# Performance work log

Measured on AMD Instinct MI355X. Metric: run time of the kernel, lower is better.

Reference implementation:

```python
import jax, jax.numpy as jnp
import numpy as np

N_NODES = 100000
N_EDGES = 3200000
IN_FEATS = 512
N_HIDDEN = 64
N_CLASSES = 16
K_HOPS = 10
ALPHA = 0.1


def setup_inputs() -> dict:
    key = jax.random.key(0)
    ks = jax.random.split(key, 6)
    feature = jax.random.normal(ks[0], (N_NODES, IN_FEATS), dtype=jnp.float32)
    W1 = jax.random.normal(ks[1], (IN_FEATS, N_HIDDEN), dtype=jnp.float32) / np.sqrt(IN_FEATS)
    b1 = jnp.zeros((N_HIDDEN,), dtype=jnp.float32)
    W2 = jax.random.normal(ks[2], (N_HIDDEN, N_CLASSES), dtype=jnp.float32) / np.sqrt(N_HIDDEN)
    b2 = jnp.zeros((N_CLASSES,), dtype=jnp.float32)
    edge_index = jax.random.randint(ks[3], (2, N_EDGES), 0, N_NODES, dtype=jnp.int64)
    # normalized edge weights ~ 1/avg_degree to keep propagation stable
    norm_A = jax.random.uniform(ks[4], (N_EDGES,), dtype=jnp.float32) * (2.0 / 32.0)
    # GPR coefficients: gamma_k = alpha*(1-alpha)^k, gamma_K = (1-alpha)^K
    kk = jnp.arange(K_HOPS + 1, dtype=jnp.float32)
    temp = ALPHA * (1.0 - ALPHA) ** kk
    temp = temp.at[-1].set((1.0 - ALPHA) ** K_HOPS)
    return {"feature": feature, "W1": W1, "b1": b1, "W2": W2, "b2": b2,
            "edge_index": edge_index, "norm_A": norm_A, "temp": temp}


def reference(feature, W1, b1, W2, b2, edge_index, norm_A, temp):
    # MLP encoder (dropout is identity in eval mode)
    h = jax.nn.relu(feature @ W1 + b1)          # [N, H]
    z = h @ W2 + b2                              # [N, C]

    src, dst = edge_index[0], edge_index[1]

    def spmm(x):
        # (norm_A @ x): gather source rows, weight, scatter-add to dest rows
        return jax.ops.segment_sum(norm_A[:, None] * x[src], dst,
                                   num_segments=N_NODES)

    hidden = temp[0] * z

    def step(carry, gamma):
        zk, hid = carry
        zk = spmm(zk)
        return (zk, hid + gamma * zk), None

    (zk, hidden), _ = jax.lax.scan(step, (z, hidden), temp[1:])
    return hidden
```

## Files before the change

### kernel.cpp

```cpp
#include <hip/hip_runtime.h>
#include <hip/hip_bf16.h>

#define NN 100000
#define NE 3200000
#define IN_F 512
#define NH 64
#define NC 16
#define K_HOPS 10

#define BSPAN 256
#define NBUCKC ((NN + BSPAN - 1) / BSPAN)
#define NBUCKP 512
#define CAP 9216
#define PART_BLOCKS 256
#define PCHUNK ((NE + PART_BLOCKS - 1) / PART_BLOCKS)

typedef short bf16x8 __attribute__((ext_vector_type(8)));
typedef float f32x4 __attribute__((ext_vector_type(4)));
typedef unsigned short u16;
typedef u16 u16x4 __attribute__((ext_vector_type(4)));

__device__ __forceinline__ short f2bf_s(float x) {
    __hip_bfloat16 b = __float2bfloat16(x);
    return *reinterpret_cast<short*>(&b);
}
__device__ __forceinline__ float bf2f_s(short s) {
    __hip_bfloat16 b = *reinterpret_cast<__hip_bfloat16*>(&s);
    return __bfloat162float(b);
}
__device__ __forceinline__ float bf2f_u(u16 s) {
    return __uint_as_float((unsigned)s << 16);
}
__device__ __forceinline__ f32x4 bf4_to_f32(u16x4 v) {
    f32x4 r;
    r[0] = __uint_as_float((unsigned)v[0] << 16);
    r[1] = __uint_as_float((unsigned)v[1] << 16);
    r[2] = __uint_as_float((unsigned)v[2] << 16);
    r[3] = __uint_as_float((unsigned)v[3] << 16);
    return r;
}
__device__ __forceinline__ u16x4 f32_to_bf4(f32x4 r) {
    u16x4 o;
    o[0] = (u16)f2bf_s(r[0]);
    o[1] = (u16)f2bf_s(r[1]);
    o[2] = (u16)f2bf_s(r[2]);
    o[3] = (u16)f2bf_s(r[3]);
    return o;
}

__device__ __forceinline__ void split8(const f32x4 a, const f32x4 b,
                                       bf16x8& hi, bf16x8& lo) {
    float x[8] = {a[0], a[1], a[2], a[3], b[0], b[1], b[2], b[3]};
#pragma unroll
    for (int j = 0; j < 8; ++j) {
        short h = f2bf_s(x[j]);
        hi[j] = h;
        lo[j] = f2bf_s(x[j] - bf2f_s(h));
    }
}

__device__ __forceinline__ f32x4 mfma3(bf16x8 ah, bf16x8 al, bf16x8 bh,
                                       bf16x8 bl, f32x4 c) {
    c = __builtin_amdgcn_mfma_f32_16x16x32_bf16(ah, bh, c, 0, 0, 0);
    c = __builtin_amdgcn_mfma_f32_16x16x32_bf16(ah, bl, c, 0, 0, 0);
    c = __builtin_amdgcn_mfma_f32_16x16x32_bf16(al, bh, c, 0, 0, 0);
    return c;
}

__global__ __launch_bounds__(256) void conv_w_kernel(
    const float* __restrict__ W1, const float* __restrict__ W2,
    short* __restrict__ w1h, short* __restrict__ w1l,
    short* __restrict__ w2h, short* __restrict__ w2l,
    int* __restrict__ gcur)
{
    int i = blockIdx.x * 256 + threadIdx.x;
    if (i < NBUCKP) gcur[i] = i * CAP;
    if (i < IN_F * NH) {
        int k = i >> 6, n = i & 63;
        float v = W1[i];
        short h = f2bf_s(v);
        w1h[n * IN_F + k] = h;
        w1l[n * IN_F + k] = f2bf_s(v - bf2f_s(h));
    } else if (i < IN_F * NH + NH * NC) {
        int j = i - IN_F * NH;
        int k = j >> 4, c = j & 15;
        float v = W2[j];
        short h = f2bf_s(v);
        w2h[c * NH + k] = h;
        w2l[c * NH + k] = f2bf_s(v - bf2f_s(h));
    }
}

__global__ __launch_bounds__(256) void encoder_mfma(
    const float* __restrict__ X,
    const short* __restrict__ w1h, const short* __restrict__ w1l,
    const short* __restrict__ w2h, const short* __restrict__ w2l,
    const float* __restrict__ b1, const float* __restrict__ b2,
    const float* __restrict__ temp,
    u16* __restrict__ z, float* __restrict__ hid)
{
    __shared__ float hs[128 * 68];
    const int t = threadIdx.x;
    const int wave = t >> 6, lane = t & 63;
    const int lm = lane & 15, kg = lane >> 4;
    const int wrow = blockIdx.x * 128 + wave * 32;

    int r0 = wrow + lm;       if (r0 > NN - 1) r0 = NN - 1;
    int r1 = wrow + 16 + lm;  if (r1 > NN - 1) r1 = NN - 1;
    const float* xp0 = X + (size_t)r0 * IN_F + kg * 8;
    const float* xp1 = X + (size_t)r1 * IN_F + kg * 8;
    const short* bhp = w1h + lm * IN_F + kg * 8;
    const short* blp = w1l + lm * IN_F + kg * 8;

    f32x4 acc[2][4];
#pragma unroll
    for (int m = 0; m < 2; ++m)
#pragma unroll
        for (int n = 0; n < 4; ++n) acc[m][n] = (f32x4){0.f, 0.f, 0.f, 0.f};

    for (int kb = 0; kb < IN_F; kb += 32) {
        bf16x8 ah0, al0, ah1, al1;
        {
            const f32x4* p0 = reinterpret_cast<const f32x4*>(xp0 + kb);
            split8(p0[0], p0[1], ah0, al0);
            const f32x4* p1 = reinterpret_cast<const f32x4*>(xp1 + kb);
            split8(p1[0], p1[1], ah1, al1);
        }
#pragma unroll
        for (int nt = 0; nt < 4; ++nt) {
            bf16x8 bh = *reinterpret_cast<const bf16x8*>(bhp + nt * 16 * IN_F + kb);
            bf16x8 bl = *reinterpret_cast<const bf16x8*>(blp + nt * 16 * IN_F + kb);
            acc[0][nt] = mfma3(ah0, al0, bh, bl, acc[0][nt]);
            acc[1][nt] = mfma3(ah1, al1, bh, bl, acc[1][nt]);
        }
    }

    float b1v[4];
#pragma unroll
    for (int nt = 0; nt < 4; ++nt) b1v[nt] = b1[nt * 16 + lm];
#pragma unroll
    for (int m = 0; m < 2; ++m)
#pragma unroll
        for (int nt = 0; nt < 4; ++nt)
#pragma unroll
            for (int r = 0; r < 4; ++r) {
                float v = acc[m][nt][r] + b1v[nt];
                v = v > 0.f ? v : 0.f;
                hs[(wave * 32 + m * 16 + kg * 4 + r) * 68 + nt * 16 + lm] = v;
            }

    f32x4 acc2[2];
    acc2[0] = (f32x4){0.f, 0.f, 0.f, 0.f};
    acc2[1] = (f32x4){0.f, 0.f, 0.f, 0.f};
#pragma unroll
    for (int kb = 0; kb < NH; kb += 32) {
        bf16x8 bh = *reinterpret_cast<const bf16x8*>(w2h + lm * NH + kb + kg * 8);
        bf16x8 bl = *reinterpret_cast<const bf16x8*>(w2l + lm * NH + kb + kg * 8);
#pragma unroll
        for (int m = 0; m < 2; ++m) {
            const f32x4* hp = reinterpret_cast<const f32x4*>(
                &hs[(wave * 32 + m * 16 + lm) * 68 + kb + kg * 8]);
            bf16x8 ah, al;
            split8(hp[0], hp[1], ah, al);
            acc2[m] = mfma3(ah, al, bh, bl, acc2[m]);
        }
    }

    const float b2v = b2[lm];
    const float t0 = temp[0];
#pragma unroll
    for (int m = 0; m < 2; ++m)
#pragma unroll
        for (int r = 0; r < 4; ++r) {
            int node = wrow + m * 16 + kg * 4 + r;
            if (node < NN) {
                float zv = acc2[m][r] + b2v;
                z[(size_t)node * NC + lm] = (u16)f2bf_s(zv);
                hid[(size_t)node * NC + lm] = t0 * zv;
            }
        }
}

__global__ __launch_bounds__(1024) void partition_kernel(
    const int* __restrict__ src, const int* __restrict__ dst,
    const float* __restrict__ w, int* __restrict__ gcur,
    int2* __restrict__ ew)
{
    __shared__ int h[16][NBUCKP];
    __shared__ int base[NBUCKP];
    __shared__ int rnk[NBUCKP];
    const int t = threadIdx.x;
    const int wid = t >> 6;
    for (int i = t; i < 16 * NBUCKP; i += 1024) ((int*)h)[i] = 0;
    __syncthreads();
    const int s = blockIdx.x * PCHUNK;
    int e = s + PCHUNK; if (e > NE) e = NE;
    for (int i = s + t; i < e; i += 1024)
        atomicAdd(&h[wid][dst[i] >> 8], 1);
    __syncthreads();
    for (int b = t; b < NBUCKP; b += 1024) {
        int tot = 0;
#pragma unroll
        for (int ww = 0; ww < 16; ++ww) tot += h[ww][b];
        base[b] = tot ? atomicAdd(&gcur[b], tot) : 0;
        rnk[b] = 0;
    }
    __syncthreads();
    for (int i = s + t; i < e; i += 1024) {
        int d = dst[i];
        int b = d >> 8;
        int r = atomicAdd(&rnk[b], 1);
        unsigned x = (unsigned)src[i] | ((unsigned)(d & 255) << 24);
        ew[base[b] + r] = make_int2((int)x, __float_as_int(w[i]));
    }
}

__global__ __launch_bounds__(256) void bucketfill_kernel(
    const int* __restrict__ gcur, const long long* __restrict__ ew,
    int* __restrict__ srcs, u16* __restrict__ wbf,
    int2* __restrict__ rowse)
{
    __shared__ long long buf[CAP];
    __shared__ int cnt[BSPAN], excl[BSPAN], rnk[BSPAN];
    const int b = blockIdx.x;
    const int base = b * CAP;
    int n = gcur[b] - base;
    if (n > CAP) n = CAP;
    const int t = threadIdx.x;
    cnt[t] = 0;
    __syncthreads();
    for (int i = t; i < n; i += 256) {
        long long v = ew[base + i];
        buf[i] = v;
        atomicAdd(&cnt[(int)((v >> 24) & 255)], 1);
    }
    __syncthreads();
    int sv = cnt[t];
    excl[t] = sv;
    __syncthreads();
    for (int off = 1; off < 256; off <<= 1) {
        int u = (t >= off) ? excl[t - off] : 0;
        __syncthreads();
        excl[t] += u;
        __syncthreads();
    }
    int myExcl = excl[t] - sv;
    __syncthreads();
    excl[t] = myExcl;
    rnk[t] = 0;
    int node = b * BSPAN + t;
    if (node < NN) rowse[node] = make_int2(base + myExcl, sv);
    __syncthreads();
    for (int i = t; i < n; i += 256) {
        long long v = buf[i];
        int d = (int)((v >> 24) & 255);
        int r = atomicAdd(&rnk[d], 1);
        int pos = base + excl[d] + r;
        srcs[pos] = (int)(v & 0x00FFFFFFll);
        wbf[pos] = (u16)f2bf_s(__int_as_float((int)((unsigned long long)v >> 32)));
    }
}

__global__ __launch_bounds__(256) void hop_kernel(
    const int2* __restrict__ rowse, const int* __restrict__ srcs,
    const u16* __restrict__ wbf, const u16* __restrict__ in,
    u16* __restrict__ out, float* __restrict__ hid,
    const float* __restrict__ temp, int k, int last)
{
    int tid = blockIdx.x * 256 + threadIdx.x;
    int d = tid >> 2, cg = tid & 3;
    if (d >= NN) return;
    int2 rs = rowse[d];
    int e = rs.x;
    const int e1 = rs.x + rs.y;
    const u16x4* inv = reinterpret_cast<const u16x4*>(in);
    f32x4 a0 = (f32x4){0.f, 0.f, 0.f, 0.f};
    f32x4 a1 = a0, a2 = a0, a3 = a0;

    for (; e < e1 && (e & 3); ++e) {
        float w = bf2f_u(wbf[e]);
        a0 += w * bf4_to_f32(inv[(size_t)srcs[e] * 4 + cg]);
    }
    for (; e + 7 < e1; e += 8) {
        int4 s4a = *reinterpret_cast<const int4*>(srcs + e);
        int4 s4b = *reinterpret_cast<const int4*>(srcs + e + 4);
        u16x4 w4a = *reinterpret_cast<const u16x4*>(wbf + e);
        u16x4 w4b = *reinterpret_cast<const u16x4*>(wbf + e + 4);
        u16x4 v0 = inv[(size_t)s4a.x * 4 + cg];
        u16x4 v1 = inv[(size_t)s4a.y * 4 + cg];
        u16x4 v2 = inv[(size_t)s4a.z * 4 + cg];
        u16x4 v3 = inv[(size_t)s4a.w * 4 + cg];
        u16x4 v4 = inv[(size_t)s4b.x * 4 + cg];
        u16x4 v5 = inv[(size_t)s4b.y * 4 + cg];
        u16x4 v6 = inv[(size_t)s4b.z * 4 + cg];
        u16x4 v7 = inv[(size_t)s4b.w * 4 + cg];
        a0 += bf2f_u(w4a[0]) * bf4_to_f32(v0);
        a1 += bf2f_u(w4a[1]) * bf4_to_f32(v1);
        a2 += bf2f_u(w4a[2]) * bf4_to_f32(v2);
        a3 += bf2f_u(w4a[3]) * bf4_to_f32(v3);
        a0 += bf2f_u(w4b[0]) * bf4_to_f32(v4);
        a1 += bf2f_u(w4b[1]) * bf4_to_f32(v5);
        a2 += bf2f_u(w4b[2]) * bf4_to_f32(v6);
        a3 += bf2f_u(w4b[3]) * bf4_to_f32(v7);
    }
    if (e + 3 < e1) {
        int4 s4a = *reinterpret_cast<const int4*>(srcs + e);
        u16x4 w4a = *reinterpret_cast<const u16x4*>(wbf + e);
        u16x4 v0 = inv[(size_t)s4a.x * 4 + cg];
        u16x4 v1 = inv[(size_t)s4a.y * 4 + cg];
        u16x4 v2 = inv[(size_t)s4a.z * 4 + cg];
        u16x4 v3 = inv[(size_t)s4a.w * 4 + cg];
        a0 += bf2f_u(w4a[0]) * bf4_to_f32(v0);
        a1 += bf2f_u(w4a[1]) * bf4_to_f32(v1);
        a2 += bf2f_u(w4a[2]) * bf4_to_f32(v2);
        a3 += bf2f_u(w4a[3]) * bf4_to_f32(v3);
        e += 4;
    }
    for (; e < e1; ++e) {
        float w = bf2f_u(wbf[e]);
        a0 += w * bf4_to_f32(inv[(size_t)srcs[e] * 4 + cg]);
    }

    f32x4 r = (a0 + a1) + (a2 + a3);
    size_t o = (size_t)d * 4 + cg;
    if (!last) reinterpret_cast<u16x4*>(out)[o] = f32_to_bf4(r);
    const float tk = temp[k];
    reinterpret_cast<f32x4*>(hid)[o] += tk * r;
}

__global__ __launch_bounds__(256) void spmm_atomic_bf16(
    const int* __restrict__ src, const int* __restrict__ dst,
    const float* __restrict__ w, const u16* __restrict__ in,
    float* __restrict__ outf)
{
    int tid = blockIdx.x * 256 + threadIdx.x;
    int e = tid >> 4, c = tid & 15;
    if (e >= NE) return;
    float v = bf2f_u(in[(size_t)src[e] * NC + c]);
    atomicAdd(&outf[(size_t)dst[e] * NC + c], w[e] * v);
}
__global__ __launch_bounds__(256) void axpy_quant_kernel(
    float* __restrict__ hid, const float* __restrict__ outf,
    u16* __restrict__ nextb, const float* __restrict__ temp, int k)
{
    int i = blockIdx.x * 256 + threadIdx.x;
    if (i < NN * NC) {
        float r = outf[i];
        hid[i] += temp[k] * r;
        nextb[i] = (u16)f2bf_s(r);
    }
}

extern "C" void kernel_launch(void* const* d_in, const int* in_sizes, int n_in,
                              void* d_out, int out_size, void* d_ws, size_t ws_size,
                              hipStream_t stream)
{
    const float* feature = (const float*)d_in[0];
    const float* W1      = (const float*)d_in[1];
    const float* b1      = (const float*)d_in[2];
    const float* W2      = (const float*)d_in[3];
    const float* b2      = (const float*)d_in[4];
    const int*   edges   = (const int*)d_in[5];
    const float* norm_A  = (const float*)d_in[6];
    const float* temp    = (const float*)d_in[7];
    const int* src = edges;
    const int* dst = edges + NE;
    float* hid = (float*)d_out;

    char* p = (char*)d_ws;
    size_t off = 0;
    auto carve = [&](size_t bytes) {
        void* r = p + off;
        off += (bytes + 255) & ~(size_t)255;
        return r;
    };
    u16*   zkA   = (u16*)carve((size_t)NN * NC * 2);
    u16*   zkB   = (u16*)carve((size_t)NN * NC * 2);
    short* w1h   = (short*)carve((size_t)IN_F * NH * 2);
    short* w1l   = (short*)carve((size_t)IN_F * NH * 2);
    short* w2h   = (short*)carve((size_t)NH * NC * 2);
    short* w2l   = (short*)carve((size_t)NH * NC * 2);
    int*   gcur  = (int*)carve((size_t)NBUCKP * 4);
    int2*  rowse = (int2*)carve((size_t)NN * 8);
    int2*  ew    = (int2*)carve((size_t)NBUCKC * CAP * 8);
    int*   srcs  = (int*)carve((size_t)NBUCKC * CAP * 4);
    u16*   wbf   = (u16*)carve((size_t)NBUCKC * CAP * 2);
    const bool useCSR = (off <= ws_size);

    conv_w_kernel<<<(IN_F * NH + NH * NC + 255) / 256, 256, 0, stream>>>(
        W1, W2, w1h, w1l, w2h, w2l, gcur);
    encoder_mfma<<<(NN + 127) / 128, 256, 0, stream>>>(
        feature, w1h, w1l, w2h, w2l, b1, b2, temp, zkA, hid);

    if (useCSR) {
        partition_kernel<<<PART_BLOCKS, 1024, 0, stream>>>(src, dst, norm_A,
                                                           gcur, ew);
        bucketfill_kernel<<<NBUCKC, 256, 0, stream>>>(
            gcur, (const long long*)ew, srcs, wbf, rowse);

        const int hopGrid = (NN * 4 + 255) / 256;
        u16* cur = zkA;
        u16* nxt = zkB;
        for (int k = 1; k <= K_HOPS; ++k) {
            hop_kernel<<<hopGrid, 256, 0, stream>>>(
                rowse, srcs, wbf, cur, nxt, hid, temp, k, k == K_HOPS);
            u16* t2 = cur; cur = nxt; nxt = t2;
        }
    } else {
        float* outf = (float*)ew;
        const int spmmGrid = (NE * NC + 255) / 256;
        const int vecGrid  = (NN * NC + 255) / 256;
        u16* cur = zkA; u16* nxt = zkB;
        for (int k = 1; k <= K_HOPS; ++k) {
            hipMemsetAsync(outf, 0, (size_t)NN * NC * 4, stream);
            spmm_atomic_bf16<<<spmmGrid, 256, 0, stream>>>(src, dst, norm_A,
                                                           cur, outf);
            axpy_quant_kernel<<<vecGrid, 256, 0, stream>>>(hid, outf, nxt,
                                                           temp, k);
            u16* t2 = cur; cur = nxt; nxt = t2;
        }
    }
}
```

Baseline: 522.2 us.

## Store every hop in bf16 and accumulate hidden in a single final pass

Each hop kernel now writes only its bf16 output into a per-hop slot of a larger buffer, instead of also doing a read-modify-write of the fp32 hidden accumulator. A new final kernel reads all ten hop results and applies the gamma-weighted sum in one pass. This removes ten fp32 hidden read/write passes and adds ten bf16 reads plus extra workspace. The gather loop is also unrolled from 8 to 16 edges per iteration to keep more loads in flight, at some register cost. The hidden sum now uses bf16-rounded hop values, including the last hop, which was previously added in fp32.

```diff
diff --git a/kernel.cpp b/kernel.cpp
--- a/kernel.cpp
+++ b/kernel.cpp
@@ -264,8 +264,7 @@
 __global__ __launch_bounds__(256) void hop_kernel(
     const int2* __restrict__ rowse, const int* __restrict__ srcs,
     const u16* __restrict__ wbf, const u16* __restrict__ in,
-    u16* __restrict__ out, float* __restrict__ hid,
-    const float* __restrict__ temp, int k, int last)
+    u16* __restrict__ out)
 {
     int tid = blockIdx.x * 256 + threadIdx.x;
     int d = tid >> 2, cg = tid & 3;
@@ -281,11 +280,15 @@
         float w = bf2f_u(wbf[e]);
         a0 += w * bf4_to_f32(inv[(size_t)srcs[e] * 4 + cg]);
     }
-    for (; e + 7 < e1; e += 8) {
+    for (; e + 15 < e1; e += 16) {
         int4 s4a = *reinterpret_cast<const int4*>(srcs + e);
         int4 s4b = *reinterpret_cast<const int4*>(srcs + e + 4);
+        int4 s4c = *reinterpret_cast<const int4*>(srcs + e + 8);
+        int4 s4d = *reinterpret_cast<const int4*>(srcs + e + 12);
         u16x4 w4a = *reinterpret_cast<const u16x4*>(wbf + e);
         u16x4 w4b = *reinterpret_cast<const u16x4*>(wbf + e + 4);
+        u16x4 w4c = *reinterpret_cast<const u16x4*>(wbf + e + 8);
+        u16x4 w4d = *reinterpret_cast<const u16x4*>(wbf + e + 12);
         u16x4 v0 = inv[(size_t)s4a.x * 4 + cg];
         u16x4 v1 = inv[(size_t)s4a.y * 4 + cg];
         u16x4 v2 = inv[(size_t)s4a.z * 4 + cg];
@@ -294,6 +297,14 @@
         u16x4 v5 = inv[(size_t)s4b.y * 4 + cg];
         u16x4 v6 = inv[(size_t)s4b.z * 4 + cg];
         u16x4 v7 = inv[(size_t)s4b.w * 4 + cg];
+        u16x4 v8 = inv[(size_t)s4c.x * 4 + cg];
+        u16x4 v9 = inv[(size_t)s4c.y * 4 + cg];
+        u16x4 va = inv[(size_t)s4c.z * 4 + cg];
+        u16x4 vb = inv[(size_t)s4c.w * 4 + cg];
+        u16x4 vc = inv[(size_t)s4d.x * 4 + cg];
+        u16x4 vd = inv[(size_t)s4d.y * 4 + cg];
+        u16x4 ve = inv[(size_t)s4d.z * 4 + cg];
+        u16x4 vf = inv[(size_t)s4d.w * 4 + cg];
         a0 += bf2f_u(w4a[0]) * bf4_to_f32(v0);
         a1 += bf2f_u(w4a[1]) * bf4_to_f32(v1);
         a2 += bf2f_u(w4a[2]) * bf4_to_f32(v2);
@@ -302,8 +313,16 @@
         a1 += bf2f_u(w4b[1]) * bf4_to_f32(v5);
         a2 += bf2f_u(w4b[2]) * bf4_to_f32(v6);
         a3 += bf2f_u(w4b[3]) * bf4_to_f32(v7);
-    }
-    if (e + 3 < e1) {
+        a0 += bf2f_u(w4c[0]) * bf4_to_f32(v8);
+        a1 += bf2f_u(w4c[1]) * bf4_to_f32(v9);
+        a2 += bf2f_u(w4c[2]) * bf4_to_f32(va);
+        a3 += bf2f_u(w4c[3]) * bf4_to_f32(vb);
+        a0 += bf2f_u(w4d[0]) * bf4_to_f32(vc);
+        a1 += bf2f_u(w4d[1]) * bf4_to_f32(vd);
+        a2 += bf2f_u(w4d[2]) * bf4_to_f32(ve);
+        a3 += bf2f_u(w4d[3]) * bf4_to_f32(vf);
+    }
+    for (; e + 3 < e1; e += 4) {
         int4 s4a = *reinterpret_cast<const int4*>(srcs + e);
         u16x4 w4a = *reinterpret_cast<const u16x4*>(wbf + e);
         u16x4 v0 = inv[(size_t)s4a.x * 4 + cg];
@@ -314,7 +333,6 @@
         a1 += bf2f_u(w4a[1]) * bf4_to_f32(v1);
         a2 += bf2f_u(w4a[2]) * bf4_to_f32(v2);
         a3 += bf2f_u(w4a[3]) * bf4_to_f32(v3);
-        e += 4;
     }
     for (; e < e1; ++e) {
         float w = bf2f_u(wbf[e]);
@@ -322,10 +340,22 @@
     }
 
     f32x4 r = (a0 + a1) + (a2 + a3);
-    size_t o = (size_t)d * 4 + cg;
-    if (!last) reinterpret_cast<u16x4*>(out)[o] = f32_to_bf4(r);
-    const float tk = temp[k];
-    reinterpret_cast<f32x4*>(hid)[o] += tk * r;
+    reinterpret_cast<u16x4*>(out)[(size_t)d * 4 + cg] = f32_to_bf4(r);
+}
+
+__global__ __launch_bounds__(256) void final_kernel(
+    const u16* __restrict__ zs, size_t zstride4,
+    float* __restrict__ hid, const float* __restrict__ temp)
+{
+    int o = blockIdx.x * 256 + threadIdx.x;
+    if (o >= NN * 4) return;
+    f32x4 h = reinterpret_cast<f32x4*>(hid)[o];
+#pragma unroll
+    for (int k = 1; k <= K_HOPS; ++k) {
+        const u16x4* zk = reinterpret_cast<const u16x4*>(zs + (size_t)k * zstride4 * 4);
+        h += temp[k] * bf4_to_f32(zk[o]);
+    }
+    reinterpret_cast<f32x4*>(hid)[o] = h;
 }
 
 __global__ __launch_bounds__(256) void spmm_atomic_bf16(
@@ -374,8 +404,9 @@
         off += (bytes + 255) & ~(size_t)255;
         return r;
     };
-    u16*   zkA   = (u16*)carve((size_t)NN * NC * 2);
-    u16*   zkB   = (u16*)carve((size_t)NN * NC * 2);
+    const size_t zelems = (size_t)NN * NC;
+    const size_t zstride = (zelems * 2 + 255) & ~(size_t)255;
+    u16*   zs    = (u16*)carve(zstride * (K_HOPS + 1));
     short* w1h   = (short*)carve((size_t)IN_F * NH * 2);
     short* w1l   = (short*)carve((size_t)IN_F * NH * 2);
     short* w2h   = (short*)carve((size_t)NH * NC * 2);
@@ -386,11 +417,12 @@
     int*   srcs  = (int*)carve((size_t)NBUCKC * CAP * 4);
     u16*   wbf   = (u16*)carve((size_t)NBUCKC * CAP * 2);
     const bool useCSR = (off <= ws_size);
+    const size_t zs4 = zstride / 2;
 
     conv_w_kernel<<<(IN_F * NH + NH * NC + 255) / 256, 256, 0, stream>>>(
         W1, W2, w1h, w1l, w2h, w2l, gcur);
     encoder_mfma<<<(NN + 127) / 128, 256, 0, stream>>>(
-        feature, w1h, w1l, w2h, w2l, b1, b2, temp, zkA, hid);
+        feature, w1h, w1l, w2h, w2l, b1, b2, temp, zs, hid);
 
     if (useCSR) {
         partition_kernel<<<PART_BLOCKS, 1024, 0, stream>>>(src, dst, norm_A,
@@ -399,18 +431,18 @@
             gcur, (const long long*)ew, srcs, wbf, rowse);
 
         const int hopGrid = (NN * 4 + 255) / 256;
-        u16* cur = zkA;
-        u16* nxt = zkB;
         for (int k = 1; k <= K_HOPS; ++k) {
             hop_kernel<<<hopGrid, 256, 0, stream>>>(
-                rowse, srcs, wbf, cur, nxt, hid, temp, k, k == K_HOPS);
-            u16* t2 = cur; cur = nxt; nxt = t2;
-        }
+                rowse, srcs, wbf, zs + (size_t)(k - 1) * zs4,
+                zs + (size_t)k * zs4);
+        }
+        final_kernel<<<hopGrid, 256, 0, stream>>>(zs, zs4 / 4, hid, temp);
     } else {
         float* outf = (float*)ew;
         const int spmmGrid = (NE * NC + 255) / 256;
         const int vecGrid  = (NN * NC + 255) / 256;
-        u16* cur = zkA; u16* nxt = zkB;
+        u16* cur = zs;
+        u16* nxt = zs + zs4;
         for (int k = 1; k <= K_HOPS; ++k) {
             hipMemsetAsync(outf, 0, (size_t)NN * NC * 4, stream);
             spmm_atomic_bf16<<<spmmGrid, 256, 0, stream>>>(src, dst, norm_A,
```

After: 537.6 us. 1.03x slower.

## Sort nodes by degree within buckets to balance hop kernel wavefronts

Applied to the files above, without the earlier changes.

Bucketfill now builds a per-bucket permutation that orders the 256 nodes of each bucket by in-degree (capped at 127) using a shared histogram and prefix scan. The hop kernel reads this order array, so the 16 nodes sharing a wavefront have similar edge counts and fewer lanes sit idle. In exchange it adds an indirection load per thread, scatters the hid and output writes (rows are no longer contiguous per wave), and adds a little preprocessing work. The int4-to-vector-type change is cosmetic.

```diff
diff --git a/kernel.cpp b/kernel.cpp
--- a/kernel.cpp
+++ b/kernel.cpp
@@ -10,6 +10,7 @@
 
 #define BSPAN 256
 #define NBUCKC ((NN + BSPAN - 1) / BSPAN)
+#define NPOS (NBUCKC * BSPAN)
 #define NBUCKP 512
 #define CAP 9216
 #define PART_BLOCKS 256
@@ -17,6 +18,7 @@
 
 typedef short bf16x8 __attribute__((ext_vector_type(8)));
 typedef float f32x4 __attribute__((ext_vector_type(4)));
+typedef int   i32x4 __attribute__((ext_vector_type(4)));
 typedef unsigned short u16;
 typedef u16 u16x4 __attribute__((ext_vector_type(4)));
 
@@ -218,16 +220,19 @@
 __global__ __launch_bounds__(256) void bucketfill_kernel(
     const int* __restrict__ gcur, const long long* __restrict__ ew,
     int* __restrict__ srcs, u16* __restrict__ wbf,
-    int2* __restrict__ rowse)
+    int2* __restrict__ rowse, int* __restrict__ order)
 {
     __shared__ long long buf[CAP];
     __shared__ int cnt[BSPAN], excl[BSPAN], rnk[BSPAN];
+    __shared__ int dhist[128], dcur[128];
     const int b = blockIdx.x;
     const int base = b * CAP;
     int n = gcur[b] - base;
     if (n > CAP) n = CAP;
     const int t = threadIdx.x;
     cnt[t] = 0;
+    order[b * BSPAN + t] = -1;
+    if (t < 128) dhist[t] = 0;
     __syncthreads();
     for (int i = t; i < n; i += 256) {
         long long v = ew[base + i];
@@ -248,8 +253,26 @@
     __syncthreads();
     excl[t] = myExcl;
     rnk[t] = 0;
-    int node = b * BSPAN + t;
-    if (node < NN) rowse[node] = make_int2(base + myExcl, sv);
+    const int node = b * BSPAN + t;
+    const bool valid = node < NN;
+    if (valid) rowse[node] = make_int2(base + myExcl, sv);
+    int dg = sv > 127 ? 127 : sv;
+    if (valid) atomicAdd(&dhist[dg], 1);
+    __syncthreads();
+    if (t < 128) dcur[t] = dhist[t];
+    __syncthreads();
+    for (int off = 1; off < 128; off <<= 1) {
+        int u = (t >= off && t < 128) ? dcur[t - off] : 0;
+        __syncthreads();
+        if (t < 128) dcur[t] += u;
+        __syncthreads();
+    }
+    if (t < 128) dcur[t] -= dhist[t];
+    __syncthreads();
+    if (valid) {
+        int pos = atomicAdd(&dcur[dg], 1);
+        order[b * BSPAN + pos] = node;
+    }
     __syncthreads();
     for (int i = t; i < n; i += 256) {
         long long v = buf[i];
@@ -262,14 +285,17 @@
 }
 
 __global__ __launch_bounds__(256) void hop_kernel(
+    const int* __restrict__ order,
     const int2* __restrict__ rowse, const int* __restrict__ srcs,
     const u16* __restrict__ wbf, const u16* __restrict__ in,
     u16* __restrict__ out, float* __restrict__ hid,
     const float* __restrict__ temp, int k, int last)
 {
     int tid = blockIdx.x * 256 + threadIdx.x;
-    int d = tid >> 2, cg = tid & 3;
-    if (d >= NN) return;
+    int idx = tid >> 2, cg = tid & 3;
+    if (idx >= NPOS) return;
+    int d = order[idx];
+    if (d < 0) return;
     int2 rs = rowse[d];
     int e = rs.x;
     const int e1 = rs.x + rs.y;
@@ -282,18 +308,18 @@
         a0 += w * bf4_to_f32(inv[(size_t)srcs[e] * 4 + cg]);
     }
     for (; e + 7 < e1; e += 8) {
-        int4 s4a = *reinterpret_cast<const int4*>(srcs + e);
-        int4 s4b = *reinterpret_cast<const int4*>(srcs + e + 4);
+        i32x4 s4a = *reinterpret_cast<const i32x4*>(srcs + e);
+        i32x4 s4b = *reinterpret_cast<const i32x4*>(srcs + e + 4);
         u16x4 w4a = *reinterpret_cast<const u16x4*>(wbf + e);
         u16x4 w4b = *reinterpret_cast<const u16x4*>(wbf + e + 4);
-        u16x4 v0 = inv[(size_t)s4a.x * 4 + cg];
-        u16x4 v1 = inv[(size_t)s4a.y * 4 + cg];
-        u16x4 v2 = inv[(size_t)s4a.z * 4 + cg];
-        u16x4 v3 = inv[(size_t)s4a.w * 4 + cg];
-        u16x4 v4 = inv[(size_t)s4b.x * 4 + cg];
-        u16x4 v5 = inv[(size_t)s4b.y * 4 + cg];
-        u16x4 v6 = inv[(size_t)s4b.z * 4 + cg];
-        u16x4 v7 = inv[(size_t)s4b.w * 4 + cg];
+        u16x4 v0 = inv[(size_t)s4a[0] * 4 + cg];
+        u16x4 v1 = inv[(size_t)s4a[1] * 4 + cg];
+        u16x4 v2 = inv[(size_t)s4a[2] * 4 + cg];
+        u16x4 v3 = inv[(size_t)s4a[3] * 4 + cg];
+        u16x4 v4 = inv[(size_t)s4b[0] * 4 + cg];
+        u16x4 v5 = inv[(size_t)s4b[1] * 4 + cg];
+        u16x4 v6 = inv[(size_t)s4b[2] * 4 + cg];
+        u16x4 v7 = inv[(size_t)s4b[3] * 4 + cg];
         a0 += bf2f_u(w4a[0]) * bf4_to_f32(v0);
         a1 += bf2f_u(w4a[1]) * bf4_to_f32(v1);
         a2 += bf2f_u(w4a[2]) * bf4_to_f32(v2);
@@ -304,12 +330,12 @@
         a3 += bf2f_u(w4b[3]) * bf4_to_f32(v7);
     }
     if (e + 3 < e1) {
-        int4 s4a = *reinterpret_cast<const int4*>(srcs + e);
+        i32x4 s4a = *reinterpret_cast<const i32x4*>(srcs + e);
         u16x4 w4a = *reinterpret_cast<const u16x4*>(wbf + e);
-        u16x4 v0 = inv[(size_t)s4a.x * 4 + cg];
-        u16x4 v1 = inv[(size_t)s4a.y * 4 + cg];
-        u16x4 v2 = inv[(size_t)s4a.z * 4 + cg];
-        u16x4 v3 = inv[(size_t)s4a.w * 4 + cg];
+        u16x4 v0 = inv[(size_t)s4a[0] * 4 + cg];
+        u16x4 v1 = inv[(size_t)s4a[1] * 4 + cg];
+        u16x4 v2 = inv[(size_t)s4a[2] * 4 + cg];
+        u16x4 v3 = inv[(size_t)s4a[3] * 4 + cg];
         a0 += bf2f_u(w4a[0]) * bf4_to_f32(v0);
         a1 += bf2f_u(w4a[1]) * bf4_to_f32(v1);
         a2 += bf2f_u(w4a[2]) * bf4_to_f32(v2);
@@ -382,6 +408,7 @@
     short* w2l   = (short*)carve((size_t)NH * NC * 2);
     int*   gcur  = (int*)carve((size_t)NBUCKP * 4);
     int2*  rowse = (int2*)carve((size_t)NN * 8);
+    int*   order = (int*)carve((size_t)NPOS * 4);
     int2*  ew    = (int2*)carve((size_t)NBUCKC * CAP * 8);
     int*   srcs  = (int*)carve((size_t)NBUCKC * CAP * 4);
     u16*   wbf   = (u16*)carve((size_t)NBUCKC * CAP * 2);
@@ -396,14 +423,14 @@
         partition_kernel<<<PART_BLOCKS, 1024, 0, stream>>>(src, dst, norm_A,
                                                            gcur, ew);
         bucketfill_kernel<<<NBUCKC, 256, 0, stream>>>(
-            gcur, (const long long*)ew, srcs, wbf, rowse);
-
-        const int hopGrid = (NN * 4 + 255) / 256;
+            gcur, (const long long*)ew, srcs, wbf, rowse, order);
+
+        const int hopGrid = (NPOS * 4) / 256;
         u16* cur = zkA;
         u16* nxt = zkB;
         for (int k = 1; k <= K_HOPS; ++k) {
             hop_kernel<<<hopGrid, 256, 0, stream>>>(
-                rowse, srcs, wbf, cur, nxt, hid, temp, k, k == K_HOPS);
+                order, rowse, srcs, wbf, cur, nxt, hid, temp, k, k == K_HOPS);
             u16* t2 = cur; cur = nxt; nxt = t2;
         }
     } else {
@@ -412,7 +439,7 @@
         const int vecGrid  = (NN * NC + 255) / 256;
         u16* cur = zkA; u16* nxt = zkB;
         for (int k = 1; k <= K_HOPS; ++k) {
-            hipMemsetAsync(outf, 0, (size_t)NN * NC * 4, stream);
+            (void)hipMemsetAsync(outf, 0, (size_t)NN * NC * 4, stream);
             spmm_atomic_bf16<<<spmmGrid, 256, 0, stream>>>(src, dst, norm_A,
                                                            cur, outf);
             axpy_quant_kernel<<<vecGrid, 256, 0, stream>>>(hid, outf, nxt,
```

Result: slower. 613.6 us (+17.5%).
